# Kernel tuning notes

Hardware: AMD Instinct MI355X
Metric: run time of the kernel (lower is better)

Reference implementation:

```python
import jax, jax.numpy as jnp
import numpy as np
import math

E = 1152          # hidden_size
H = 16            # num_attention_heads
HD = E // H       # 72 head_dim
HD2 = HD // 2     # 36 differential half head dim
FF = 4304         # intermediate_size
B, S = 32, 256
LAYER_IDX = 12
LAMBDA_INIT = 0.8 - 0.6 * math.exp(-0.3 * (LAYER_IDX - 1))
RMS_EPS = 1e-6
SUBLN_EPS = 1e-5


def _rms_norm(x, w, eps):
    var = jnp.mean(jnp.square(x), axis=-1, keepdims=True)
    return x * jax.lax.rsqrt(var + eps) * w


def setup_inputs() -> dict:
    key = jax.random.key(0)
    ks = jax.random.split(key, 16)
    lin = lambda k, o, i: jax.random.normal(k, (o, i), jnp.float32) * 0.02
    return {
        "hidden_states": jax.random.normal(ks[0], (B, S, E), jnp.float32),
        "Wq": lin(ks[1], E, E), "bq": jnp.zeros((E,), jnp.float32),
        "Wk": lin(ks[2], E, E), "bk": jnp.zeros((E,), jnp.float32),
        "Wv": lin(ks[3], E, E), "bv": jnp.zeros((E,), jnp.float32),
        "Wo": lin(ks[4], E, E), "bo": jnp.zeros((E,), jnp.float32),
        "lq1": jax.random.normal(ks[5], (HD2,), jnp.float32) * 0.1,
        "lk1": jax.random.normal(ks[6], (HD2,), jnp.float32) * 0.1,
        "lq2": jax.random.normal(ks[7], (HD2,), jnp.float32) * 0.1,
        "lk2": jax.random.normal(ks[8], (HD2,), jnp.float32) * 0.1,
        "subln_w": jnp.ones((HD,), jnp.float32),
        "rms1_w": jnp.ones((E,), jnp.float32),
        "rms2_w": jnp.ones((E,), jnp.float32),
        "fc1_w": lin(ks[9], FF, E), "fc1_b": jnp.zeros((FF,), jnp.float32),
        "fc2_w": lin(ks[10], E, FF), "fc2_b": jnp.zeros((E,), jnp.float32),
    }


def reference(hidden_states, Wq, bq, Wk, bk, Wv, bv, Wo, bo,
              lq1, lk1, lq2, lk2, subln_w, rms1_w, rms2_w,
              fc1_w, fc1_b, fc2_w, fc2_b):
    residual = hidden_states
    x = _rms_norm(hidden_states, rms1_w, RMS_EPS)

    # projections
    q = x @ Wq.T + bq
    k = x @ Wk.T + bk
    v = x @ Wv.T + bv
    # dual head split: [B, 2H, S, HD2] for q,k; [B, H, S, HD] for v
    q = q.reshape(B, S, 2 * H, HD2).transpose(0, 2, 1, 3)
    k = k.reshape(B, S, 2 * H, HD2).transpose(0, 2, 1, 3)
    v = v.reshape(B, S, H, HD).transpose(0, 2, 1, 3)

    # note: scale uses full head_dim (faithful to source)
    aw = jnp.einsum('bhqd,bhkd->bhqk', q, k) / math.sqrt(HD)
    aw = jnp.nan_to_num(aw)
    aw = jax.nn.softmax(aw.astype(jnp.float32), axis=-1).astype(q.dtype)

    lambda_full = (jnp.exp(jnp.sum(lq1 * lk1)) - jnp.exp(jnp.sum(lq2 * lk2))
                   + LAMBDA_INIT).astype(q.dtype)
    aw = aw.reshape(B, H, 2, S, S)
    aw = aw[:, :, 0] - lambda_full * aw[:, :, 1]  # [B, H, S, S]

    attn = jnp.einsum('bhqk,bhkd->bhqd', aw, v)   # [B, H, S, HD]
    attn = _rms_norm(attn, subln_w, SUBLN_EPS) * (1.0 - LAMBDA_INIT)
    attn = attn.transpose(0, 2, 1, 3).reshape(B, S, E)
    attn = attn @ Wo.T + bo

    h = residual + attn

    residual = h
    y = _rms_norm(h, rms2_w, RMS_EPS)
    y = jax.nn.gelu(y @ fc1_w.T + fc1_b, approximate=True)
    y = y @ fc2_w.T + fc2_b
    return residual + y
```

## Files before the change

### kernel.cpp

```cpp
#include <hip/hip_runtime.h>
#include <hip/hip_bf16.h>

typedef __hip_bfloat16 bf16;
typedef __attribute__((ext_vector_type(4))) float f32x4;
typedef __attribute__((ext_vector_type(8))) __bf16 bf16x8;

constexpr int kE   = 1152;
constexpr int kH   = 16;
constexpr int kHD2 = 36;
constexpr int kFF  = 4304;
constexpr int kFFP = 4352;
constexpr int kB   = 32;
constexpr int kS   = 256;
constexpr int kT   = kB * kS;
constexpr int kQKV = 3456;
constexpr float kLambdaInit = 0.7778701f;
constexpr float kRmsEps = 1e-6f;
constexpr float kSublnEps = 1e-5f;

__device__ inline void async_copy16(const void* gsrc, void* ldst) {
    __builtin_amdgcn_global_load_lds(
        (__attribute__((address_space(1))) void*)gsrc,
        (__attribute__((address_space(3))) void*)ldst, 16, 0, 0);
}

constexpr int  kNEE  = kE * kE;
constexpr long kSeg0 = 3L * kNEE;
constexpr long kSeg1 = kSeg0 + kNEE;
constexpr long kSeg2 = kSeg1 + (long)kFFP * kE;
constexpr long kCvtTotal = kSeg2 + (long)kE * kFFP;

__global__ __launch_bounds__(256) void convert_all(
    const float* __restrict__ Wq, const float* __restrict__ Wk,
    const float* __restrict__ Wv, const float* __restrict__ Wo,
    const float* __restrict__ f1, const float* __restrict__ f2,
    bf16* __restrict__ wqkv, bf16* __restrict__ wo,
    bf16* __restrict__ w1, bf16* __restrict__ w2)
{
    long i = ((long)blockIdx.x * 256 + threadIdx.x) * 4;
    if (i >= kCvtTotal) return;
    float4 v = make_float4(0.f, 0.f, 0.f, 0.f);
    bf16* dst;
    if (i < kSeg0) {
        long j = i;
        const float* src = (j < kNEE) ? Wq : (j < 2L * kNEE) ? Wk : Wv;
        v = *(const float4*)(src + (j % kNEE));
        dst = wqkv + j;
    } else if (i < kSeg1) {
        long j = i - kSeg0;
        v = *(const float4*)(Wo + j);
        dst = wo + j;
    } else if (i < kSeg2) {
        long j = i - kSeg1;
        if (j < (long)kFF * kE) v = *(const float4*)(f1 + j);
        dst = w1 + j;
    } else {
        long j = i - kSeg2;
        int n = (int)(j / kFFP), k = (int)(j - (long)n * kFFP);
        if (k < kFF) v = *(const float4*)(f2 + (long)n * kFF + k);
        dst = w2 + j;
    }
    union { uint2 u; bf16 e[4]; } o;
    o.e[0] = __float2bfloat16(v.x); o.e[1] = __float2bfloat16(v.y);
    o.e[2] = __float2bfloat16(v.z); o.e[3] = __float2bfloat16(v.w);
    *(uint2*)dst = o.u;
}

__global__ __launch_bounds__(256) void prep_bias(
    const float* __restrict__ bq, const float* __restrict__ bk,
    const float* __restrict__ bv, const float* __restrict__ fb,
    float* __restrict__ bqkv, float* __restrict__ fbp)
{
    int i = blockIdx.x * 256 + threadIdx.x;
    if (i < kQKV) {
        float v = (i < kE) ? bq[i] : (i < 2 * kE) ? bk[i - kE] : bv[i - 2 * kE];
        bqkv[i] = v;
    }
    if (i < kFFP) fbp[i] = (i < kFF) ? fb[i] : 0.f;
}

__global__ __launch_bounds__(256) void rmsnorm_kernel(
    const float* __restrict__ x, const float* __restrict__ w,
    bf16* __restrict__ out, float eps)
{
    int row = blockIdx.x;
    const float* xr = x + (size_t)row * kE;
    float vals[5];
    float ss = 0.f;
    int n = 0;
    for (int j = threadIdx.x; j < kE; j += 256) {
        float v = xr[j];
        vals[n++] = v;
        ss += v * v;
    }
    for (int m = 32; m > 0; m >>= 1) ss += __shfl_xor(ss, m, 64);
    __shared__ float red[4];
    if ((threadIdx.x & 63) == 0) red[threadIdx.x >> 6] = ss;
    __syncthreads();
    float tot = red[0] + red[1] + red[2] + red[3];
    float scale = rsqrtf(tot / (float)kE + eps);
    n = 0;
    for (int j = threadIdx.x; j < kE; j += 256)
        out[(size_t)row * kE + j] = __float2bfloat16(vals[n++] * scale * w[j]);
}

#define GBAR() do { asm volatile("" ::: "memory"); \
                    __builtin_amdgcn_s_barrier();  \
                    asm volatile("" ::: "memory"); } while (0)

template <int EPI>
__global__ __launch_bounds__(256, 3) void gemm128(
    const bf16* __restrict__ A, const bf16* __restrict__ Bw,
    const float* __restrict__ bias, const float* add, void* out,
    int N, int K, int ldk)
{
    __shared__ __align__(16) char sm[2][24576];

    const int tid  = threadIdx.x;
    const int lane = tid & 63;
    const int wave = tid >> 6;
    const int wm   = wave >> 1;
    const int wn   = wave & 1;
    const int q4   = lane >> 4;
    const int l16  = lane & 15;

    const int orig = blockIdx.y * gridDim.x + blockIdx.x;
    const int xcd  = orig & 7;
    const int loc  = orig >> 3;
    const int bm   = xcd * 8 + (loc & 7);
    const int bn   = loc >> 3;

    const int NT = K >> 6;

    const int trow = tid >> 3;
    const int tswz = ((tid & 7) ^ (trow & 7)) << 4;
    const size_t rs = (size_t)ldk * 2;
    const char* aG = (const char*)A + (size_t)(bm * 128 + trow) * rs + tswz;
    const char* bG = (const char*)Bw + (size_t)(bn * 64 + trow) * rs + tswz;

#define STAGE(par, tt)                                                          \
    {                                                                           \
        const size_t kb = (size_t)(tt) * 128;                                   \
        async_copy16(aG + kb,           sm[par] + tid * 16);                    \
        async_copy16(aG + 32 * rs + kb, sm[par] + tid * 16 + 4096);             \
        async_copy16(aG + 64 * rs + kb, sm[par] + tid * 16 + 8192);             \
        async_copy16(aG + 96 * rs + kb, sm[par] + tid * 16 + 12288);            \
        async_copy16(bG + kb,           sm[par] + tid * 16 + 16384);            \
        async_copy16(bG + 32 * rs + kb, sm[par] + tid * 16 + 20480);            \
    }

    int aoff[2], boff[2];
#pragma unroll
    for (int kh = 0; kh < 2; ++kh) {
        const int sw = (((kh << 2) + q4) ^ (l16 & 7)) << 4;
        aoff[kh] = (wm * 64 + l16) * 128 + sw;
        boff[kh] = 16384 + (wn * 32 + l16) * 128 + sw;
    }

    f32x4 acc[4][2] = {};
    bf16x8 afr[4][2], bfr[2][2];

    STAGE(0, 0);
    if (NT > 1) {
        STAGE(1, 1);
        asm volatile("s_waitcnt vmcnt(6)" ::: "memory");
    } else {
        asm volatile("s_waitcnt vmcnt(0)" ::: "memory");
    }
    GBAR();

    for (int t = 0; t < NT; ++t) {
        const int par = t & 1;
        const char* sB0 = sm[par];

#pragma unroll
        for (int mi = 0; mi < 4; ++mi)
#pragma unroll
            for (int kh = 0; kh < 2; ++kh)
                afr[mi][kh] = *(const bf16x8*)(sB0 + mi * 2048 + aoff[kh]);
#pragma unroll
        for (int ni = 0; ni < 2; ++ni)
#pragma unroll
            for (int kh = 0; kh < 2; ++kh)
                bfr[ni][kh] = *(const bf16x8*)(sB0 + ni * 2048 + boff[kh]);
        asm volatile("s_waitcnt lgkmcnt(0)" ::: "memory");
        GBAR();

        if (t + 2 < NT) STAGE(par, t + 2);
        __builtin_amdgcn_s_setprio(1);
#pragma unroll
        for (int mi = 0; mi < 4; ++mi)
#pragma unroll
            for (int ni = 0; ni < 2; ++ni)
#pragma unroll
                for (int kh = 0; kh < 2; ++kh)
                    acc[mi][ni] = __builtin_amdgcn_mfma_f32_16x16x32_bf16(
                        afr[mi][kh], bfr[ni][kh], acc[mi][ni], 0, 0, 0);
        __builtin_amdgcn_s_setprio(0);
        if (t + 2 < NT) {
            asm volatile("s_waitcnt vmcnt(6)" ::: "memory");
        } else {
            asm volatile("s_waitcnt vmcnt(0)" ::: "memory");
        }
        GBAR();
    }
#undef STAGE

    const int growb = bm * 128 + wm * 64;
    const int gcolb = bn * 64 + wn * 32;
#pragma unroll
    for (int mi = 0; mi < 4; ++mi) {
#pragma unroll
        for (int ni = 0; ni < 2; ++ni) {
            const int gcol = gcolb + ni * 16 + l16;
            const float bv = bias[gcol];
#pragma unroll
            for (int r = 0; r < 4; ++r) {
                const int grow = growb + mi * 16 + q4 * 4 + r;
                float v = acc[mi][ni][r] + bv;
                size_t idx = (size_t)grow * N + gcol;
                if (EPI == 0) {
                    ((bf16*)out)[idx] = __float2bfloat16(v);
                } else if (EPI == 1) {
                    float u = 1.5957691216f * (v + 0.044715f * v * v * v);
                    float g = v / (1.f + __expf(-u));
                    ((bf16*)out)[idx] = __float2bfloat16(g);
                } else {
                    ((float*)out)[idx] = v + add[idx];
                }
            }
        }
    }
}

union U8 { bf16x8 v; uint4 u4; uint2 u2[2]; unsigned short e[8]; };

__global__ __launch_bounds__(256) void attn_mfma(
    const bf16* __restrict__ qkv,
    const float* __restrict__ lq1, const float* __restrict__ lk1,
    const float* __restrict__ lq2, const float* __restrict__ lk2,
    const float* __restrict__ subln_w, bf16* __restrict__ out)
{
    __shared__ __align__(16) bf16 Kp[256 * 136];
    __shared__ __align__(16) bf16 VT[80 * 264];
    __shared__ __align__(16) bf16 Pb[4 * 16 * 264];

    const int tid = threadIdx.x;
    const int h = blockIdx.x & 15;
    const int b = blockIdx.x >> 4;
    const size_t tokbase = (size_t)b * kS;

    float s1 = 0.f, s2 = 0.f;
    for (int i = 0; i < kHD2; ++i) { s1 += lq1[i] * lk1[i]; s2 += lq2[i] * lk2[i]; }
    const float lam = __expf(s1) - __expf(s2) + kLambdaInit;

    for (int c = tid; c < 256 * 34; c += 256) {
        int row = c / 34, s4 = (c - row * 34) * 4;
        uint2 val = make_uint2(0u, 0u);
        const bf16* kg = qkv + (tokbase + row) * kQKV + kE + h * 72;
        if (s4 < 36)                    val = *(const uint2*)(kg + s4);
        else if (s4 >= 64 && s4 < 100)  val = *(const uint2*)(kg + s4 - 28);
        *(uint2*)(Kp + row * 136 + s4) = val;
    }
    for (int c = tid; c < 256 * 18; c += 256) {
        int j = c / 18, s4 = (c - j * 18) * 4;
        union { uint2 u; unsigned short e[4]; } uu;
        uu.u = *(const uint2*)(qkv + (tokbase + j) * kQKV + 2 * kE + h * 72 + s4);
#pragma unroll
        for (int x = 0; x < 4; ++x)
            ((unsigned short*)VT)[(s4 + x) * 264 + j] = uu.e[x];
    }
    for (int c = tid; c < 8 * 256; c += 256) {
        int d = 72 + (c >> 8), j = c & 255;
        ((unsigned short*)VT)[d * 264 + j] = 0;
    }
    __syncthreads();

    const int w = tid >> 6, lane = tid & 63, quad = lane >> 4, l16 = lane & 15;
    bf16* Pw = Pb + w * (16 * 264);
    const float sc = 0.117851130f;
    const float oscale = 1.f - kLambdaInit;

    float sw[5];
#pragma unroll
    for (int dt = 0; dt < 5; ++dt) {
        int d = dt * 16 + l16;
        sw[dt] = (d < 72) ? subln_w[d] : 0.f;
    }

    for (int s = 0; s < 4; ++s) {
        const int q0 = w * 64 + s * 16;
        const bf16* qg = qkv + (tokbase + q0 + l16) * kQKV + h * 72;
        U8 qe0, qe1, qo0, qo1;
        qe0.u4 = *(const uint4*)(qg + quad * 8);
        qe1.u4 = *(const uint4*)(qg + 32);
        qo0.u2[0] = *(const uint2*)(qg + 36 + quad * 8);
        qo0.u2[1] = *(const uint2*)(qg + 40 + quad * 8);
        qo1.u2[0] = *(const uint2*)(qg + 68);
        qo1.u2[1] = *(const uint2*)(qg + 72);
#pragma unroll
        for (int j = 0; j < 8; ++j) {
            bool keep = (quad == 0) && (j < 4);
            if (!keep) { qe1.e[j] = 0; qo1.e[j] = 0; }
        }

        f32x4 se[16], so[16];
#pragma unroll
        for (int t = 0; t < 16; ++t) { se[t] = f32x4{0,0,0,0}; so[t] = f32x4{0,0,0,0}; }
#pragma unroll
        for (int t = 0; t < 16; ++t) {
            const bf16* kr = Kp + (t * 16 + l16) * 136;
            bf16x8 ke0 = *(const bf16x8*)(kr + quad * 8);
            bf16x8 ke1 = *(const bf16x8*)(kr + 32 + quad * 8);
            bf16x8 ko0 = *(const bf16x8*)(kr + 64 + quad * 8);
            bf16x8 ko1 = *(const bf16x8*)(kr + 96 + quad * 8);
            se[t] = __builtin_amdgcn_mfma_f32_16x16x32_bf16(qe0.v, ke0, se[t], 0, 0, 0);
            se[t] = __builtin_amdgcn_mfma_f32_16x16x32_bf16(qe1.v, ke1, se[t], 0, 0, 0);
            so[t] = __builtin_amdgcn_mfma_f32_16x16x32_bf16(qo0.v, ko0, so[t], 0, 0, 0);
            so[t] = __builtin_amdgcn_mfma_f32_16x16x32_bf16(qo1.v, ko1, so[t], 0, 0, 0);
        }

#pragma unroll
        for (int reg = 0; reg < 4; ++reg) {
            float me = -1e30f, mo = -1e30f;
#pragma unroll
            for (int t = 0; t < 16; ++t) {
                me = fmaxf(me, se[t][reg]);
                mo = fmaxf(mo, so[t][reg]);
            }
#pragma unroll
            for (int m = 1; m < 16; m <<= 1) {
                me = fmaxf(me, __shfl_xor(me, m, 64));
                mo = fmaxf(mo, __shfl_xor(mo, m, 64));
            }
            float sume = 0.f, sumo = 0.f;
#pragma unroll
            for (int t = 0; t < 16; ++t) {
                float pe = __expf((se[t][reg] - me) * sc);
                float po = __expf((so[t][reg] - mo) * sc);
                se[t][reg] = pe; sume += pe;
                so[t][reg] = po; sumo += po;
            }
#pragma unroll
            for (int m = 1; m < 16; m <<= 1) {
                sume += __shfl_xor(sume, m, 64);
                sumo += __shfl_xor(sumo, m, 64);
            }
            const float ie = 1.f / sume, io = lam / sumo;
            bf16* prow = Pw + (quad * 4 + reg) * 264;
#pragma unroll
            for (int t = 0; t < 16; ++t) {
                float p = se[t][reg] * ie - so[t][reg] * io;
                prow[t * 16 + l16] = __float2bfloat16(p);
            }
        }

        f32x4 oacc[5];
#pragma unroll
        for (int dt = 0; dt < 5; ++dt) oacc[dt] = f32x4{0,0,0,0};
#pragma unroll
        for (int k0 = 0; k0 < 256; k0 += 32) {
            bf16x8 pf = *(const bf16x8*)(Pw + l16 * 264 + k0 + quad * 8);
#pragma unroll
            for (int dt = 0; dt < 5; ++dt) {
                bf16x8 vf = *(const bf16x8*)(VT + (dt * 16 + l16) * 264 + k0 + quad * 8);
                oacc[dt] = __builtin_amdgcn_mfma_f32_16x16x32_bf16(pf, vf, oacc[dt], 0, 0, 0);
            }
        }

#pragma unroll
        for (int reg = 0; reg < 4; ++reg) {
            float ssq = 0.f;
#pragma unroll
            for (int dt = 0; dt < 5; ++dt) {
                float v = oacc[dt][reg];
                if (dt < 4 || l16 < 8) ssq += v * v;
            }
#pragma unroll
            for (int m = 1; m < 16; m <<= 1) ssq += __shfl_xor(ssq, m, 64);
            float scale = rsqrtf(ssq * (1.f / 72.f) + kSublnEps) * oscale;
            size_t orow = (tokbase + q0 + quad * 4 + reg) * (size_t)kE + h * 72;
#pragma unroll
            for (int dt = 0; dt < 5; ++dt) {
                int d = dt * 16 + l16;
                if (d < 72)
                    out[orow + d] = __float2bfloat16(oacc[dt][reg] * scale * sw[dt]);
            }
        }
    }
}

extern "C" void kernel_launch(void* const* d_in, const int* in_sizes, int n_in,
                              void* d_out, int out_size, void* d_ws, size_t ws_size,
                              hipStream_t stream)
{
    const float* hidden = (const float*)d_in[0];
    const float* Wq = (const float*)d_in[1];
    const float* bq = (const float*)d_in[2];
    const float* Wk = (const float*)d_in[3];
    const float* bk = (const float*)d_in[4];
    const float* Wv = (const float*)d_in[5];
    const float* bv = (const float*)d_in[6];
    const float* Wo = (const float*)d_in[7];
    const float* bo = (const float*)d_in[8];
    const float* lq1 = (const float*)d_in[9];
    const float* lk1 = (const float*)d_in[10];
    const float* lq2 = (const float*)d_in[11];
    const float* lk2 = (const float*)d_in[12];
    const float* subln_w = (const float*)d_in[13];
    const float* rms1_w = (const float*)d_in[14];
    const float* rms2_w = (const float*)d_in[15];
    const float* fc1_w = (const float*)d_in[16];
    const float* fc1_b = (const float*)d_in[17];
    const float* fc2_w = (const float*)d_in[18];
    const float* fc2_b = (const float*)d_in[19];
    float* outp = (float*)d_out;

    char* wsp = (char*)d_ws;
    size_t off = 0;
    auto alloc = [&](size_t bytes) {
        char* p = wsp + off;
        off += (bytes + 255) & ~(size_t)255;
        return p;
    };
    bf16* wqkv = (bf16*)alloc((size_t)kQKV * kE * 2);
    bf16* wo   = (bf16*)alloc((size_t)kE * kE * 2);
    bf16* w1   = (bf16*)alloc((size_t)kFFP * kE * 2);
    bf16* w2   = (bf16*)alloc((size_t)kE * kFFP * 2);
    float* bqkv = (float*)alloc((size_t)kQKV * 4);
    float* b1   = (float*)alloc((size_t)kFFP * 4);
    bf16* xb    = (bf16*)alloc((size_t)kT * kE * 2);
    bf16* big   = (bf16*)alloc((size_t)kT * kFFP * 2);
    (void)ws_size;

    convert_all<<<(int)((kCvtTotal / 4 + 255) / 256), 256, 0, stream>>>(
        Wq, Wk, Wv, Wo, fc1_w, fc2_w, wqkv, wo, w1, w2);
    prep_bias<<<17, 256, 0, stream>>>(bq, bk, bv, fc1_b, bqkv, b1);

    rmsnorm_kernel<<<kT, 256, 0, stream>>>(hidden, rms1_w, xb, kRmsEps);
    gemm128<0><<<dim3(kQKV / 64, kT / 128), 256, 0, stream>>>(
        xb, wqkv, bqkv, nullptr, big, kQKV, kE, kE);
    attn_mfma<<<kB * kH, 256, 0, stream>>>(
        big, lq1, lk1, lq2, lk2, subln_w, xb);
    gemm128<2><<<dim3(kE / 64, kT / 128), 256, 0, stream>>>(
        xb, wo, bo, hidden, d_out, kE, kE, kE);
    rmsnorm_kernel<<<kT, 256, 0, stream>>>(outp, rms2_w, xb, kRmsEps);
    gemm128<1><<<dim3(kFFP / 64, kT / 128), 256, 0, stream>>>(
        xb, w1, b1, nullptr, big, kFFP, kE, kE);
    gemm128<2><<<dim3(kE / 64, kT / 128), 256, 0, stream>>>(
        big, w2, fc2_b, outp, d_out, kE, kFFP, kFFP);
}
```

Before: 642.0 us.

## Widen GEMM tile to 128x128 with single-buffered A and double-buffered B

```diff
diff --git a/kernel.cpp b/kernel.cpp
--- a/kernel.cpp
+++ b/kernel.cpp
@@ -114,7 +114,7 @@
     const float* __restrict__ bias, const float* add, void* out,
     int N, int K, int ldk)
 {
-    __shared__ __align__(16) char sm[2][24576];
+    __shared__ __align__(16) char sm[49152];
 
     const int tid  = threadIdx.x;
     const int lane = tid & 63;
@@ -136,17 +136,24 @@
     const int tswz = ((tid & 7) ^ (trow & 7)) << 4;
     const size_t rs = (size_t)ldk * 2;
     const char* aG = (const char*)A + (size_t)(bm * 128 + trow) * rs + tswz;
-    const char* bG = (const char*)Bw + (size_t)(bn * 64 + trow) * rs + tswz;
-
-#define STAGE(par, tt)                                                          \
+    const char* bG = (const char*)Bw + (size_t)(bn * 128 + trow) * rs + tswz;
+
+#define STAGE_A(tt)                                                             \
     {                                                                           \
         const size_t kb = (size_t)(tt) * 128;                                   \
-        async_copy16(aG + kb,           sm[par] + tid * 16);                    \
-        async_copy16(aG + 32 * rs + kb, sm[par] + tid * 16 + 4096);             \
-        async_copy16(aG + 64 * rs + kb, sm[par] + tid * 16 + 8192);             \
-        async_copy16(aG + 96 * rs + kb, sm[par] + tid * 16 + 12288);            \
-        async_copy16(bG + kb,           sm[par] + tid * 16 + 16384);            \
-        async_copy16(bG + 32 * rs + kb, sm[par] + tid * 16 + 20480);            \
+        async_copy16(aG + kb,           sm + tid * 16);                         \
+        async_copy16(aG + 32 * rs + kb, sm + tid * 16 + 4096);                  \
+        async_copy16(aG + 64 * rs + kb, sm + tid * 16 + 8192);                  \
+        async_copy16(aG + 96 * rs + kb, sm + tid * 16 + 12288);                 \
+    }
+#define STAGE_B(par, tt)                                                        \
+    {                                                                           \
+        const size_t kb = (size_t)(tt) * 128;                                   \
+        char* d = sm + 16384 + (par) * 16384 + tid * 16;                        \
+        async_copy16(bG + kb,           d);                                     \
+        async_copy16(bG + 32 * rs + kb, d + 4096);                              \
+        async_copy16(bG + 64 * rs + kb, d + 8192);                              \
+        async_copy16(bG + 96 * rs + kb, d + 12288);                             \
     }
 
     int aoff[2], boff[2];
@@ -154,16 +161,17 @@
     for (int kh = 0; kh < 2; ++kh) {
         const int sw = (((kh << 2) + q4) ^ (l16 & 7)) << 4;
         aoff[kh] = (wm * 64 + l16) * 128 + sw;
-        boff[kh] = 16384 + (wn * 32 + l16) * 128 + sw;
-    }
-
-    f32x4 acc[4][2] = {};
-    bf16x8 afr[4][2], bfr[2][2];
-
-    STAGE(0, 0);
+        boff[kh] = (wn * 64 + l16) * 128 + sw;
+    }
+
+    f32x4 acc[4][4] = {};
+    bf16x8 afr[4][2], bfr[4][2];
+
+    STAGE_A(0);
+    STAGE_B(0, 0);
     if (NT > 1) {
-        STAGE(1, 1);
-        asm volatile("s_waitcnt vmcnt(6)" ::: "memory");
+        STAGE_B(1, 1);
+        asm volatile("s_waitcnt vmcnt(4)" ::: "memory");
     } else {
         asm volatile("s_waitcnt vmcnt(0)" ::: "memory");
     }
@@ -171,47 +179,49 @@
 
     for (int t = 0; t < NT; ++t) {
         const int par = t & 1;
-        const char* sB0 = sm[par];
+        const char* sB = sm + 16384 + par * 16384;
 
 #pragma unroll
         for (int mi = 0; mi < 4; ++mi)
 #pragma unroll
             for (int kh = 0; kh < 2; ++kh)
-                afr[mi][kh] = *(const bf16x8*)(sB0 + mi * 2048 + aoff[kh]);
-#pragma unroll
-        for (int ni = 0; ni < 2; ++ni)
+                afr[mi][kh] = *(const bf16x8*)(sm + mi * 2048 + aoff[kh]);
+#pragma unroll
+        for (int ni = 0; ni < 4; ++ni)
 #pragma unroll
             for (int kh = 0; kh < 2; ++kh)
-                bfr[ni][kh] = *(const bf16x8*)(sB0 + ni * 2048 + boff[kh]);
+                bfr[ni][kh] = *(const bf16x8*)(sB + ni * 2048 + boff[kh]);
         asm volatile("s_waitcnt lgkmcnt(0)" ::: "memory");
         GBAR();
 
-        if (t + 2 < NT) STAGE(par, t + 2);
+        if (t + 1 < NT) STAGE_A(t + 1);
+        if (t + 2 < NT) STAGE_B(par, t + 2);
         __builtin_amdgcn_s_setprio(1);
 #pragma unroll
         for (int mi = 0; mi < 4; ++mi)
 #pragma unroll
-            for (int ni = 0; ni < 2; ++ni)
+            for (int ni = 0; ni < 4; ++ni)
 #pragma unroll
                 for (int kh = 0; kh < 2; ++kh)
                     acc[mi][ni] = __builtin_amdgcn_mfma_f32_16x16x32_bf16(
                         afr[mi][kh], bfr[ni][kh], acc[mi][ni], 0, 0, 0);
         __builtin_amdgcn_s_setprio(0);
         if (t + 2 < NT) {
-            asm volatile("s_waitcnt vmcnt(6)" ::: "memory");
+            asm volatile("s_waitcnt vmcnt(4)" ::: "memory");
         } else {
             asm volatile("s_waitcnt vmcnt(0)" ::: "memory");
         }
         GBAR();
     }
-#undef STAGE
+#undef STAGE_A
+#undef STAGE_B
 
     const int growb = bm * 128 + wm * 64;
-    const int gcolb = bn * 64 + wn * 32;
+    const int gcolb = bn * 128 + wn * 64;
 #pragma unroll
     for (int mi = 0; mi < 4; ++mi) {
 #pragma unroll
-        for (int ni = 0; ni < 2; ++ni) {
+        for (int ni = 0; ni < 4; ++ni) {
             const int gcol = gcolb + ni * 16 + l16;
             const float bv = bias[gcol];
 #pragma unroll
@@ -438,15 +448,15 @@
     prep_bias<<<17, 256, 0, stream>>>(bq, bk, bv, fc1_b, bqkv, b1);
 
     rmsnorm_kernel<<<kT, 256, 0, stream>>>(hidden, rms1_w, xb, kRmsEps);
-    gemm128<0><<<dim3(kQKV / 64, kT / 128), 256, 0, stream>>>(
+    gemm128<0><<<dim3(kQKV / 128, kT / 128), 256, 0, stream>>>(
         xb, wqkv, bqkv, nullptr, big, kQKV, kE, kE);
     attn_mfma<<<kB * kH, 256, 0, stream>>>(
         big, lq1, lk1, lq2, lk2, subln_w, xb);
-    gemm128<2><<<dim3(kE / 64, kT / 128), 256, 0, stream>>>(
+    gemm128<2><<<dim3(kE / 128, kT / 128), 256, 0, stream>>>(
         xb, wo, bo, hidden, d_out, kE, kE, kE);
     rmsnorm_kernel<<<kT, 256, 0, stream>>>(outp, rms2_w, xb, kRmsEps);
-    gemm128<1><<<dim3(kFFP / 64, kT / 128), 256, 0, stream>>>(
+    gemm128<1><<<dim3(kFFP / 128, kT / 128), 256, 0, stream>>>(
         xb, w1, b1, nullptr, big, kFFP, kE, kE);
-    gemm128<2><<<dim3(kE / 64, kT / 128), 256, 0, stream>>>(
+    gemm128<2><<<dim3(kE / 128, kT / 128), 256, 0, stream>>>(
         big, w2, fc2_b, outp, d_out, kE, kFFP, kFFP);
 }
```

After: 616.7 us. 3.9% less time.
